# Kernel tuning notes

Hardware: AMD Instinct MI355X
Metric: run time of the kernel (lower is better)

The kernel has to match this reference:

```python
import jax, jax.numpy as jnp
import numpy as np

DIM = 512
NUM_HEADS = 8
HEAD_DIM = DIM // NUM_HEADS
SCALE = HEAD_DIM ** (-0.5)
EPS = 1e-12  # torch F.normalize eps


def setup_inputs() -> dict:
    key = jax.random.key(0)
    ks = jax.random.split(key, 6)
    B, C, H, W = 8, DIM, 64, 64
    x = jax.random.normal(ks[0], (B, C, H, W), dtype=jnp.float32)
    mask = jax.random.uniform(ks[1], (B, 1, H, W), dtype=jnp.float32)
    s = DIM ** -0.5
    Wq = jax.random.normal(ks[2], (DIM, DIM), dtype=jnp.float32) * s
    Wk = jax.random.normal(ks[3], (DIM, DIM), dtype=jnp.float32) * s
    Wv = jax.random.normal(ks[4], (DIM, DIM), dtype=jnp.float32) * s
    Wp = jax.random.normal(ks[5], (DIM, DIM), dtype=jnp.float32) * s
    return {"x": x, "mask": mask, "Wq": Wq, "Wk": Wk, "Wv": Wv, "Wp": Wp}


def _split_heads(t, B, HW):
    # [B, HW, C] -> [B, heads, head_dim, HW]
    return t.reshape(B, HW, NUM_HEADS, HEAD_DIM).transpose(0, 2, 3, 1)


def _l2norm(t):
    # torch F.normalize: x / max(||x||, eps) along last axis
    n = jnp.sqrt(jnp.sum(t * t, axis=-1, keepdims=True))
    return t / jnp.maximum(n, EPS)


def reference(x, mask, Wq, Wk, Wv, Wp):
    B, C, H, W = x.shape
    HW = H * W
    xm = x * mask                             # masked input for q, k
    # NCHW -> [B, HW, C]
    xt = x.transpose(0, 2, 3, 1).reshape(B, HW, C)
    xmt = xm.transpose(0, 2, 3, 1).reshape(B, HW, C)
    q = _split_heads(xmt @ Wq.T, B, HW)       # [B, h, d, HW]
    k = _split_heads(xmt @ Wk.T, B, HW)
    v = _split_heads(xt @ Wv.T, B, HW)
    q = _l2norm(q)
    k = _l2norm(k)
    # channel-wise attention: [B, h, d, d]
    attn = jnp.einsum('bhcn,bhdn->bhcd', q, k) * SCALE
    attn = jax.nn.softmax(attn, axis=-1)
    out = jnp.einsum('bhcd,bhdn->bhcn', attn, v)  # [B, h, d, HW]
    out = out.transpose(0, 3, 1, 2).reshape(B, HW, C)  # [B, HW, C]
    out = out @ Wp.T
    return out.reshape(B, H, W, C).transpose(0, 3, 1, 2)  # NCHW
```

## Files before the change

kernel.cpp:

```cpp
#include <hip/hip_runtime.h>
#include <math.h>

#define DIMC 512
#define HW 4096
#define SCALE 0.125f
#define EPSN 1e-12f

typedef __attribute__((ext_vector_type(8))) short bf16x8;
typedef __attribute__((ext_vector_type(4))) float f32x4;

__device__ __forceinline__ unsigned short f2bf(float f) {
    union { float f; unsigned int u; } v; v.f = f;
    unsigned int u = v.u;
    return (unsigned short)((u + 0x7fffu + ((u >> 16) & 1u)) >> 16);
}
__device__ __forceinline__ float bf2f(unsigned short h) {
    union { unsigned int u; float f; } v; v.u = ((unsigned int)h) << 16;
    return v.f;
}

union Pack8 { int4 v; unsigned short u[8]; };

__device__ __forceinline__ void gload_lds16(const unsigned short* src, char* ldst) {
    __builtin_amdgcn_global_load_lds(
        (const __attribute__((address_space(1))) void*)src,
        (__attribute__((address_space(3))) void*)ldst, 16, 0, 0);
}

__global__ __launch_bounds__(256) void convert_w(
    const float* __restrict__ Wq, const float* __restrict__ Wk,
    unsigned short* __restrict__ Wb)
{
    int i = (blockIdx.x * 256 + threadIdx.x) * 4;
    const float* s = (i < 262144) ? Wq : Wk;
    int off = i & 262143;
    float4 v4 = *(const float4*)(s + off);
    ushort4 o;
    o.x = f2bf(v4.x); o.y = f2bf(v4.y); o.z = f2bf(v4.z); o.w = f2bf(v4.w);
    *(ushort4*)(Wb + i) = o;
}

__global__ __launch_bounds__(256) void wvt_conv(
    const float* __restrict__ Wv, unsigned short* __restrict__ WvT)
{
    const int cp0 = blockIdx.y * 64;
    const int c30 = blockIdx.x * 64;
    __shared__ unsigned short sT[64][65];
    const int t = threadIdx.x;
    #pragma unroll
    for (int i = 0; i < 4; ++i) {
        int ch = t + i * 256;
        int r = ch >> 4, col4 = (ch & 15) * 4;
        float4 v4 = *(const float4*)(Wv + (size_t)(cp0 + r) * DIMC + c30 + col4);
        sT[r][col4 + 0] = f2bf(v4.x); sT[r][col4 + 1] = f2bf(v4.y);
        sT[r][col4 + 2] = f2bf(v4.z); sT[r][col4 + 3] = f2bf(v4.w);
    }
    __syncthreads();
    #pragma unroll
    for (int i = 0; i < 2; ++i) {
        int ch = t + i * 256;
        int n = ch >> 3, cc = (ch & 7) * 8;
        Pack8 pk;
        #pragma unroll
        for (int e = 0; e < 8; ++e) pk.u[e] = sT[cc + e][n];
        *(int4*)(WvT + (size_t)(c30 + n) * DIMC + cp0 + cc) = pk.v;
    }
}

__global__ __launch_bounds__(256) void prep_x(
    const float* __restrict__ x, const float* __restrict__ mask,
    unsigned short* __restrict__ xT, unsigned short* __restrict__ xmb)
{
    const int b  = blockIdx.z;
    const int c0 = blockIdx.y * 64;
    const int n0 = blockIdx.x * 64;
    __shared__ unsigned short sT[64][65];
    const int t = threadIdx.x;
    #pragma unroll
    for (int i = 0; i < 4; ++i) {
        int ch = t + i * 256;
        int r = ch >> 4, col4 = (ch & 15) * 4;
        float4 v4 = *(const float4*)(x + ((size_t)b * DIMC + c0 + r) * HW + n0 + col4);
        sT[r][col4 + 0] = f2bf(v4.x); sT[r][col4 + 1] = f2bf(v4.y);
        sT[r][col4 + 2] = f2bf(v4.z); sT[r][col4 + 3] = f2bf(v4.w);
        float4 mv = *(const float4*)(mask + (size_t)b * HW + n0 + col4);
        ushort4 xm;
        xm.x = f2bf(v4.x * mv.x); xm.y = f2bf(v4.y * mv.y);
        xm.z = f2bf(v4.z * mv.z); xm.w = f2bf(v4.w * mv.w);
        *(ushort4*)(xmb + ((size_t)b * DIMC + c0 + r) * HW + n0 + col4) = xm;
    }
    __syncthreads();
    #pragma unroll
    for (int i = 0; i < 2; ++i) {
        int ch = t + i * 256;
        int n = ch >> 3, cc = (ch & 7) * 8;
        Pack8 pk;
        #pragma unroll
        for (int e = 0; e < 8; ++e) pk.u[e] = sT[cc + e][n];
        *(int4*)(xT + ((size_t)b * HW + n0 + n) * DIMC + c0 + cc) = pk.v;
    }
}

__global__ __launch_bounds__(256) void gram_mfma(
    const unsigned short* __restrict__ xmb, unsigned short* __restrict__ G)
{
    const int b   = blockIdx.z;
    const int cA0 = blockIdx.y * 64;
    const int cB0 = blockIdx.x * 128;
    const unsigned short* A = xmb + (size_t)b * DIMC * HW + (size_t)cA0 * HW;
    const unsigned short* B = xmb + (size_t)b * DIMC * HW + (size_t)cB0 * HW;

    __shared__ __align__(16) char sm[49152];

    const int t = threadIdx.x, lane = t & 63, w = t >> 6;
    const int wm = w >> 1, wn = w & 1;
    const int rsub = lane >> 3;
    const int srccol = ((lane & 7) ^ rsub) << 3;

    f32x4 zero = {0.f, 0.f, 0.f, 0.f};
    f32x4 acc[2][4];
    #pragma unroll
    for (int m = 0; m < 2; ++m)
        #pragma unroll
        for (int n = 0; n < 4; ++n) acc[m][n] = zero;

    #define STAGE_G(buf, c0)                                                  \
        {                                                                     \
            char* dst = sm + (buf) * 24576;                                   \
            _Pragma("unroll")                                                 \
            for (int i = 0; i < 2; ++i) {                                     \
                int ii = w * 2 + i;                                           \
                gload_lds16(A + (size_t)(ii * 8 + rsub) * HW + (c0) + srccol, \
                            dst + ii * 1024);                                 \
            }                                                                 \
            _Pragma("unroll")                                                 \
            for (int i = 0; i < 4; ++i) {                                     \
                int ii = w * 4 + i;                                           \
                gload_lds16(B + (size_t)(ii * 8 + rsub) * HW + (c0) + srccol, \
                            dst + 8192 + ii * 1024);                          \
            }                                                                 \
        }

    STAGE_G(0, 0);
    int cur = 0;
    for (int c0 = 0; c0 < HW; c0 += 64) {
        __syncthreads();
        if (c0 + 64 < HW) STAGE_G(cur ^ 1, c0 + 64);
        const char* sA = sm + cur * 24576;
        const char* sB = sA + 8192;
        #pragma unroll
        for (int s = 0; s < 2; ++s) {
            bf16x8 af[2], bfr[4];
            #pragma unroll
            for (int m = 0; m < 2; ++m) {
                int r = wm * 32 + m * 16 + (lane & 15);
                int byte = r * 128 + s * 64 + ((lane >> 4) << 4);
                byte ^= (r & 7) << 4;
                af[m] = *(const bf16x8*)(sA + byte);
            }
            #pragma unroll
            for (int n = 0; n < 4; ++n) {
                int r = wn * 64 + n * 16 + (lane & 15);
                int byte = r * 128 + s * 64 + ((lane >> 4) << 4);
                byte ^= (r & 7) << 4;
                bfr[n] = *(const bf16x8*)(sB + byte);
            }
            #pragma unroll
            for (int m = 0; m < 2; ++m)
                #pragma unroll
                for (int n = 0; n < 4; ++n)
                    acc[m][n] = __builtin_amdgcn_mfma_f32_16x16x32_bf16(
                        af[m], bfr[n], acc[m][n], 0, 0, 0);
        }
        cur ^= 1;
    }
    #undef STAGE_G

    unsigned short* st = (unsigned short*)sm;
    __syncthreads();
    #pragma unroll
    for (int m = 0; m < 2; ++m)
        #pragma unroll
        for (int n = 0; n < 4; ++n)
            #pragma unroll
            for (int r4 = 0; r4 < 4; ++r4) {
                int jl = wm * 32 + m * 16 + ((lane >> 4) << 2) + r4;
                int nl = wn * 64 + n * 16 + (lane & 15);
                st[jl * 136 + nl] = f2bf(acc[m][n][r4]);
            }
    __syncthreads();
    #pragma unroll
    for (int it = 0; it < 4; ++it) {
        int idx = t + it * 256, jl = idx >> 4, l16 = idx & 15;
        int4 pv = *(int4*)((char*)sm + jl * 272 + l16 * 16);
        *(int4*)(G + ((size_t)b * DIMC + cA0 + jl) * DIMC + cB0 + l16 * 8) = pv;
    }
}

__global__ __launch_bounds__(256) void gemm_nn_128(
    const unsigned short* __restrict__ Ag, size_t aBatch,
    const unsigned short* __restrict__ Bg, size_t bBatch,
    unsigned short* __restrict__ Cg, size_t cBatch)
{
    const int b  = blockIdx.z;
    const int j0 = blockIdx.y * 128;
    const int n0 = blockIdx.x * 128;
    const unsigned short* A = Ag + (size_t)b * aBatch + (size_t)j0 * DIMC;
    const unsigned short* B = Bg + (size_t)b * bBatch + (size_t)n0 * DIMC;

    __shared__ __align__(16) char sm[65536];

    const int t = threadIdx.x, lane = t & 63, w = t >> 6;
    const int wm = w >> 1, wn = w & 1;
    const int rsub = lane >> 3;
    const int srccol = ((lane & 7) ^ rsub) << 3;

    f32x4 zero = {0.f, 0.f, 0.f, 0.f};
    f32x4 acc[4][4];
    #pragma unroll
    for (int m = 0; m < 4; ++m)
        #pragma unroll
        for (int n = 0; n < 4; ++n) acc[m][n] = zero;

    #define STAGE_NN(buf, c0)                                                   \
        {                                                                       \
            char* dst = sm + (buf) * 32768;                                     \
            _Pragma("unroll")                                                   \
            for (int i = 0; i < 4; ++i) {                                       \
                int ii = w * 4 + i;                                             \
                gload_lds16(A + (size_t)(ii * 8 + rsub) * DIMC + (c0) + srccol, \
                            dst + ii * 1024);                                   \
                gload_lds16(B + (size_t)(ii * 8 + rsub) * DIMC + (c0) + srccol, \
                            dst + 16384 + ii * 1024);                           \
            }                                                                   \
        }

    STAGE_NN(0, 0);
    int cur = 0;
    for (int c0 = 0; c0 < DIMC; c0 += 64) {
        __syncthreads();
        if (c0 + 64 < DIMC) STAGE_NN(cur ^ 1, c0 + 64);
        const char* sA = sm + cur * 32768;
        const char* sB = sA + 16384;
        #pragma unroll
        for (int s = 0; s < 2; ++s) {
            bf16x8 af[4], bfr[4];
            #pragma unroll
            for (int m = 0; m < 4; ++m) {
                int r = wm * 64 + m * 16 + (lane & 15);
                int byte = r * 128 + s * 64 + ((lane >> 4) << 4);
                byte ^= (r & 7) << 4;
                af[m] = *(const bf16x8*)(sA + byte);
            }
            #pragma unroll
            for (int n = 0; n < 4; ++n) {
                int r = wn * 64 + n * 16 + (lane & 15);
                int byte = r * 128 + s * 64 + ((lane >> 4) << 4);
                byte ^= (r & 7) << 4;
                bfr[n] = *(const bf16x8*)(sB + byte);
            }
            #pragma unroll
            for (int m = 0; m < 4; ++m)
                #pragma unroll
                for (int n = 0; n < 4; ++n)
                    acc[m][n] = __builtin_amdgcn_mfma_f32_16x16x32_bf16(
                        af[m], bfr[n], acc[m][n], 0, 0, 0);
        }
        cur ^= 1;
    }
    #undef STAGE_NN

    unsigned short* st = (unsigned short*)sm;
    __syncthreads();
    #pragma unroll
    for (int m = 0; m < 4; ++m)
        #pragma unroll
        for (int n = 0; n < 4; ++n)
            #pragma unroll
            for (int r4 = 0; r4 < 4; ++r4) {
                int jl = wm * 64 + m * 16 + ((lane >> 4) << 2) + r4;
                int nl = wn * 64 + n * 16 + (lane & 15);
                st[jl * 136 + nl] = f2bf(acc[m][n][r4]);
            }
    __syncthreads();
    #pragma unroll
    for (int it = 0; it < 8; ++it) {
        int idx = t + it * 256, jl = idx >> 4, l16 = idx & 15;
        int4 pv = *(int4*)((char*)sm + jl * 272 + l16 * 16);
        *(int4*)(Cg + (size_t)b * cBatch + (size_t)(j0 + jl) * DIMC + n0 + l16 * 8) = pv;
    }
}

__global__ __launch_bounds__(256) void sumsq_dot(
    const unsigned short* __restrict__ TU, const unsigned short* __restrict__ Wb,
    float* __restrict__ sumsq)
{
    const int row  = blockIdx.x * 4 + (threadIdx.x >> 6);
    const int lane = threadIdx.x & 63;
    const int b = row >> 10, jj = row & 1023;
    Pack8 a, wv;
    a.v  = *(const int4*)(TU + ((size_t)b * 1024 + jj) * DIMC + lane * 8);
    wv.v = *(const int4*)(Wb + (size_t)jj * DIMC + lane * 8);
    float s = 0.f;
    #pragma unroll
    for (int e = 0; e < 8; ++e) s = fmaf(bf2f(a.u[e]), bf2f(wv.u[e]), s);
    #pragma unroll
    for (int o = 32; o > 0; o >>= 1) s += __shfl_down(s, o, 64);
    if (lane == 0)
        sumsq[(jj >> 9) * 4096 + b * DIMC + (jj & 511)] = s;
}

__global__ __launch_bounds__(256) void s_softmax(
    const unsigned short* __restrict__ TU, const unsigned short* __restrict__ Wb,
    const float* __restrict__ sumsq, float* __restrict__ attn)
{
    const int bh = blockIdx.x;
    const int b = bh >> 3, h = bh & 7;
    const unsigned short* A = TU + ((size_t)b * 1024 + h * 64) * DIMC;
    const unsigned short* B = Wb + 262144 + (size_t)(h * 64) * DIMC;

    __shared__ __align__(16) char sm[32768];
    __shared__ float sS[64][65];
    __shared__ float srk[64];

    const int t = threadIdx.x, lane = t & 63, w = t >> 6;
    const int wm = w >> 1, wn = w & 1;
    const int rsub = lane >> 3;
    const int srccol = ((lane & 7) ^ rsub) << 3;

    f32x4 zero = {0.f, 0.f, 0.f, 0.f};
    f32x4 acc[2][2];
    #pragma unroll
    for (int m = 0; m < 2; ++m)
        #pragma unroll
        for (int n = 0; n < 2; ++n) acc[m][n] = zero;

    #define STAGE_S(buf, c0)                                                    \
        {                                                                       \
            char* dst = sm + (buf) * 16384;                                     \
            _Pragma("unroll")                                                   \
            for (int i = 0; i < 2; ++i) {                                       \
                int ii = w * 2 + i;                                             \
                gload_lds16(A + (size_t)(ii * 8 + rsub) * DIMC + (c0) + srccol, \
                            dst + ii * 1024);                                   \
                gload_lds16(B + (size_t)(ii * 8 + rsub) * DIMC + (c0) + srccol, \
                            dst + 8192 + ii * 1024);                            \
            }                                                                   \
        }

    STAGE_S(0, 0);
    int cur = 0;
    for (int c0 = 0; c0 < DIMC; c0 += 64) {
        __syncthreads();
        if (c0 + 64 < DIMC) STAGE_S(cur ^ 1, c0 + 64);
        const char* sA = sm + cur * 16384;
        const char* sB = sA + 8192;
        #pragma unroll
        for (int s = 0; s < 2; ++s) {
            bf16x8 aq[2], bk[2];
            #pragma unroll
            for (int m = 0; m < 2; ++m) {
                int r = wm * 32 + m * 16 + (lane & 15);
                int byte = r * 128 + s * 64 + ((lane >> 4) << 4);
                byte ^= (r & 7) << 4;
                aq[m] = *(const bf16x8*)(sA + byte);
            }
            #pragma unroll
            for (int n = 0; n < 2; ++n) {
                int r = wn * 32 + n * 16 + (lane & 15);
                int byte = r * 128 + s * 64 + ((lane >> 4) << 4);
                byte ^= (r & 7) << 4;
                bk[n] = *(const bf16x8*)(sB + byte);
            }
            #pragma unroll
            for (int m = 0; m < 2; ++m)
                #pragma unroll
                for (int n = 0; n < 2; ++n)
                    acc[m][n] = __builtin_amdgcn_mfma_f32_16x16x32_bf16(
                        aq[m], bk[n], acc[m][n], 0, 0, 0);
        }
        cur ^= 1;
    }
    #undef STAGE_S

    #pragma unroll
    for (int m = 0; m < 2; ++m)
        #pragma unroll
        for (int n = 0; n < 2; ++n)
            #pragma unroll
            for (int r4 = 0; r4 < 4; ++r4) {
                int r = wm * 32 + m * 16 + ((lane >> 4) << 2) + r4;
                int c = wn * 32 + n * 16 + (lane & 15);
                sS[r][c] = acc[m][n][r4];
            }
    if (t < 64)
        srk[t] = 1.0f / fmaxf(sqrtf(sumsq[4096 + b * DIMC + h * 64 + t]), EPSN);
    __syncthreads();

    const int r = t >> 2;
    const int p = t & 3;
    const float rq = 1.0f / fmaxf(sqrtf(sumsq[b * DIMC + h * 64 + r]), EPSN);
    float row[16];
    #pragma unroll
    for (int c = 0; c < 16; ++c)
        row[c] = sS[r][p * 16 + c] * SCALE * rq * srk[p * 16 + c];
    float mx = row[0];
    #pragma unroll
    for (int c = 1; c < 16; ++c) mx = fmaxf(mx, row[c]);
    mx = fmaxf(mx, __shfl_xor(mx, 1, 4));
    mx = fmaxf(mx, __shfl_xor(mx, 2, 4));
    float sum = 0.f;
    #pragma unroll
    for (int c = 0; c < 16; ++c) { row[c] = __expf(row[c] - mx); sum += row[c]; }
    sum += __shfl_xor(sum, 1, 4);
    sum += __shfl_xor(sum, 2, 4);
    const float inv = 1.0f / sum;
    float* Ao = attn + ((size_t)bh << 12) + r * 64 + p * 16;
    #pragma unroll
    for (int c4 = 0; c4 < 4; ++c4) {
        float4 o = make_float4(row[c4*4+0]*inv, row[c4*4+1]*inv,
                               row[c4*4+2]*inv, row[c4*4+3]*inv);
        *(float4*)(Ao + c4 * 4) = o;
    }
}

__global__ __launch_bounds__(256) void build_wp2(
    const float* __restrict__ Wp, const float* __restrict__ attn,
    unsigned short* __restrict__ Wp2b)
{
    const int jt = blockIdx.x;
    const int h  = blockIdx.y;
    const int b  = blockIdx.z;

    __shared__ float sA[64][64];
    __shared__ float sW[64][64];

    const int t = threadIdx.x;
    {
        const float* A = attn + ((size_t)(b * 8 + h) << 12);
        for (int i = t * 4; i < 4096; i += 1024)
            *(float4*)&sA[0][i] = *(const float4*)(A + i);
    }
    {
        const int j  = t >> 2;
        const int c0 = (t & 3) * 16;
        #pragma unroll
        for (int i = 0; i < 4; ++i) {
            float4 w4 = *(const float4*)(Wp + (size_t)(jt * 64 + j) * DIMC + h * 64 + c0 + i * 4);
            sW[c0 + i * 4 + 0][j] = w4.x; sW[c0 + i * 4 + 1][j] = w4.y;
            sW[c0 + i * 4 + 2][j] = w4.z; sW[c0 + i * 4 + 3][j] = w4.w;
        }
    }
    __syncthreads();

    const int tx = t & 15, ty = t >> 4;
    float acc[4][4] = {};
    #pragma unroll 16
    for (int c = 0; c < 64; ++c) {
        float wf[4], af[4];
        #pragma unroll
        for (int i = 0; i < 4; ++i) { wf[i] = sW[c][ty * 4 + i]; af[i] = sA[c][tx * 4 + i]; }
        #pragma unroll
        for (int r = 0; r < 4; ++r)
            #pragma unroll
            for (int cc = 0; cc < 4; ++cc)
                acc[r][cc] = fmaf(wf[r], af[cc], acc[r][cc]);
    }

    unsigned short* O = Wp2b + ((size_t)b * DIMC + jt * 64 + ty * 4) * DIMC + h * 64 + tx * 4;
    #pragma unroll
    for (int r = 0; r < 4; ++r) {
        ushort4 o4;
        o4.x = f2bf(acc[r][0]); o4.y = f2bf(acc[r][1]);
        o4.z = f2bf(acc[r][2]); o4.w = f2bf(acc[r][3]);
        *(ushort4*)(O + (size_t)r * DIMC) = o4;
    }
}

__global__ __launch_bounds__(256) void final_mfma(
    const unsigned short* __restrict__ Wfb, const unsigned short* __restrict__ xT,
    float* __restrict__ out)
{
    const int b  = blockIdx.z;
    const int j0 = blockIdx.y * 128;
    const int n0 = blockIdx.x * 128;
    const unsigned short* A = Wfb + (size_t)b * DIMC * DIMC + (size_t)j0 * DIMC;
    const unsigned short* B = xT + (size_t)b * HW * DIMC + (size_t)n0 * DIMC;

    __shared__ __align__(16) char sm[65536];

    const int t = threadIdx.x, lane = t & 63, w = t >> 6;
    const int wm = w >> 1, wn = w & 1;
    const int rsub = lane >> 3;
    const int srccol = ((lane & 7) ^ rsub) << 3;

    f32x4 zero = {0.f, 0.f, 0.f, 0.f};
    f32x4 acc[4][4];
    #pragma unroll
    for (int m = 0; m < 4; ++m)
        #pragma unroll
        for (int n = 0; n < 4; ++n) acc[m][n] = zero;

    #define STAGE_FIN(buf, c0)                                                  \
        {                                                                       \
            char* dst = sm + (buf) * 32768;                                     \
            _Pragma("unroll")                                                   \
            for (int i = 0; i < 4; ++i) {                                       \
                int ii = w * 4 + i;                                             \
                gload_lds16(A + (size_t)(ii * 8 + rsub) * DIMC + (c0) + srccol, \
                            dst + ii * 1024);                                   \
                gload_lds16(B + (size_t)(ii * 8 + rsub) * DIMC + (c0) + srccol, \
                            dst + 16384 + ii * 1024);                           \
            }                                                                   \
        }

    STAGE_FIN(0, 0);
    int cur = 0;
    for (int c0 = 0; c0 < DIMC; c0 += 64) {
        __syncthreads();
        if (c0 + 64 < DIMC) STAGE_FIN(cur ^ 1, c0 + 64);
        const char* sA = sm + cur * 32768;
        const char* sB = sA + 16384;
        #pragma unroll
        for (int s = 0; s < 2; ++s) {
            bf16x8 af[4], bfr[4];
            #pragma unroll
            for (int m = 0; m < 4; ++m) {
                int r = wm * 64 + m * 16 + (lane & 15);
                int byte = r * 128 + s * 64 + ((lane >> 4) << 4);
                byte ^= (r & 7) << 4;
                af[m] = *(const bf16x8*)(sA + byte);
            }
            #pragma unroll
            for (int n = 0; n < 4; ++n) {
                int r = wn * 64 + n * 16 + (lane & 15);
                int byte = r * 128 + s * 64 + ((lane >> 4) << 4);
                byte ^= (r & 7) << 4;
                bfr[n] = *(const bf16x8*)(sB + byte);
            }
            #pragma unroll
            for (int m = 0; m < 4; ++m)
                #pragma unroll
                for (int n = 0; n < 4; ++n)
                    acc[m][n] = __builtin_amdgcn_mfma_f32_16x16x32_bf16(
                        af[m], bfr[n], acc[m][n], 0, 0, 0);
        }
        cur ^= 1;
    }
    #undef STAGE_FIN

    #pragma unroll
    for (int m = 0; m < 4; ++m)
        #pragma unroll
        for (int r4 = 0; r4 < 4; ++r4) {
            int j = j0 + wm * 64 + m * 16 + ((lane >> 4) << 2) + r4;
            size_t rowbase = ((size_t)b * DIMC + j) * HW + n0 + wn * 64 + (lane & 15);
            #pragma unroll
            for (int n = 0; n < 4; ++n)
                out[rowbase + n * 16] = acc[m][n][r4];
        }
}

extern "C" void kernel_launch(void* const* d_in, const int* in_sizes, int n_in,
                              void* d_out, int out_size, void* d_ws, size_t ws_size,
                              hipStream_t stream)
{
    const float* x    = (const float*)d_in[0];
    const float* mask = (const float*)d_in[1];
    const float* Wq   = (const float*)d_in[2];
    const float* Wk   = (const float*)d_in[3];
    const float* Wv   = (const float*)d_in[4];
    const float* Wp   = (const float*)d_in[5];
    float* out = (float*)d_out;
    char* wsb = (char*)d_ws;

    unsigned short* xT   = (unsigned short*)(wsb + 0);
    unsigned short* xmb  = (unsigned short*)(wsb + 67108864);
    unsigned short* Wb   = (unsigned short*)(wsb + 134217728);
    unsigned short* WvT  = (unsigned short*)(wsb + 135266304);
    unsigned short* G    = (unsigned short*)(wsb + 135790592);
    unsigned short* TU   = (unsigned short*)(wsb + 139984896);
    float* sumsq         = (float*)(wsb + 148373504);
    float* attn          = (float*)(wsb + 148406272);
    unsigned short* Wp2b = (unsigned short*)(wsb + 149454848);
    unsigned short* Wfb  = (unsigned short*)(wsb + 153649152);

    convert_w  <<<512,             256, 0, stream>>>(Wq, Wk, Wb);
    wvt_conv   <<<dim3(8, 8),      256, 0, stream>>>(Wv, WvT);
    prep_x     <<<dim3(64, 8, 8),  256, 0, stream>>>(x, mask, xT, xmb);
    gram_mfma  <<<dim3(4, 8, 8),   256, 0, stream>>>(xmb, G);
    gemm_nn_128<<<dim3(4, 8, 8),   256, 0, stream>>>(Wb, (size_t)0, G, (size_t)(DIMC*DIMC), TU, (size_t)(1024*DIMC));
    sumsq_dot  <<<2048,            256, 0, stream>>>(TU, Wb, sumsq);
    s_softmax  <<<64,              256, 0, stream>>>(TU, Wb, sumsq, attn);
    build_wp2  <<<dim3(8, 8, 8),   256, 0, stream>>>(Wp, attn, Wp2b);
    gemm_nn_128<<<dim3(4, 4, 8),   256, 0, stream>>>(Wp2b, (size_t)(DIMC*DIMC), WvT, (size_t)0, Wfb, (size_t)(DIMC*DIMC));
    final_mfma <<<dim3(32, 4, 8),  256, 0, stream>>>(Wfb, xT, out);
}
```

Baseline: 132.4 us.

## Split Gram-matrix reduction over HW into four partials with a reduce kernel

The Gram kernel now splits the 4096-long reduction dimension into four 1024-long chunks and enlarges the output tile to 128x128, giving 512 blocks instead of 256. Each block writes fp32 partial results, and a new reduce kernel sums the four partials and converts them to bf16. The aim is better occupancy of the compute units and more reuse of each loaded tile. The cost is an extra kernel launch, 32 MB of fp32 partial writes and reads, and uncoalesced per-element partial stores.

New measurement: 134.1 us. About the same (+1.3%).

```diff
diff --git a/kernel.cpp b/kernel.cpp
--- a/kernel.cpp
+++ b/kernel.cpp
@@ -102,15 +102,16 @@
 }
 
 __global__ __launch_bounds__(256) void gram_mfma(
-    const unsigned short* __restrict__ xmb, unsigned short* __restrict__ G)
-{
-    const int b   = blockIdx.z;
-    const int cA0 = blockIdx.y * 64;
+    const unsigned short* __restrict__ xmb, float* __restrict__ Gpart)
+{
+    const int b   = blockIdx.z & 7;
+    const int sp  = blockIdx.z >> 3;
+    const int cA0 = blockIdx.y * 128;
     const int cB0 = blockIdx.x * 128;
-    const unsigned short* A = xmb + (size_t)b * DIMC * HW + (size_t)cA0 * HW;
-    const unsigned short* B = xmb + (size_t)b * DIMC * HW + (size_t)cB0 * HW;
-
-    __shared__ __align__(16) char sm[49152];
+    const unsigned short* A = xmb + (size_t)b * DIMC * HW + (size_t)cA0 * HW + sp * 1024;
+    const unsigned short* B = xmb + (size_t)b * DIMC * HW + (size_t)cB0 * HW + sp * 1024;
+
+    __shared__ __align__(16) char sm[65536];
 
     const int t = threadIdx.x, lane = t & 63, w = t >> 6;
     const int wm = w >> 1, wn = w & 1;
@@ -118,42 +119,38 @@
     const int srccol = ((lane & 7) ^ rsub) << 3;
 
     f32x4 zero = {0.f, 0.f, 0.f, 0.f};
-    f32x4 acc[2][4];
-    #pragma unroll
-    for (int m = 0; m < 2; ++m)
+    f32x4 acc[4][4];
+    #pragma unroll
+    for (int m = 0; m < 4; ++m)
         #pragma unroll
         for (int n = 0; n < 4; ++n) acc[m][n] = zero;
 
     #define STAGE_G(buf, c0)                                                  \
         {                                                                     \
-            char* dst = sm + (buf) * 24576;                                   \
-            _Pragma("unroll")                                                 \
-            for (int i = 0; i < 2; ++i) {                                     \
-                int ii = w * 2 + i;                                           \
-                gload_lds16(A + (size_t)(ii * 8 + rsub) * HW + (c0) + srccol, \
-                            dst + ii * 1024);                                 \
-            }                                                                 \
+            char* dst = sm + (buf) * 32768;                                   \
             _Pragma("unroll")                                                 \
             for (int i = 0; i < 4; ++i) {                                     \
                 int ii = w * 4 + i;                                           \
+                gload_lds16(A + (size_t)(ii * 8 + rsub) * HW + (c0) + srccol, \
+                            dst + ii * 1024);                                 \
                 gload_lds16(B + (size_t)(ii * 8 + rsub) * HW + (c0) + srccol, \
-                            dst + 8192 + ii * 1024);                          \
+                            dst + 16384 + ii * 1024);                         \
             }                                                                 \
         }
 
     STAGE_G(0, 0);
     int cur = 0;
-    for (int c0 = 0; c0 < HW; c0 += 64) {
+    for (int c0 = 0; c0 < 1024; c0 += 64) {
         __syncthreads();
-        if (c0 + 64 < HW) STAGE_G(cur ^ 1, c0 + 64);
-        const char* sA = sm + cur * 24576;
-        const char* sB = sA + 8192;
+        if (c0 + 64 < 1024) STAGE_G(cur ^ 1, c0 + 64);
+        const char* sA = sm + cur * 32768;
+        const char* sB = sA + 16384;
         #pragma unroll
         for (int s = 0; s < 2; ++s) {
-            bf16x8 af[2], bfr[4];
-            #pragma unroll
-            for (int m = 0; m < 2; ++m) {
-                int r = wm * 32 + m * 16 + (lane & 15);
+            bf16x8 af[4], bfr[4];
+            #pragma unroll
+            for (int m = 0; m < 4; ++m) {
+                int r = wm * 64 + m * 16 + (lane & 15);
                 int byte = r * 128 + s * 64 + ((lane >> 4) << 4);
                 byte ^= (r & 7) << 4;
                 af[m] = *(const bf16x8*)(sA + byte);
@@ -166,7 +163,7 @@
                 bfr[n] = *(const bf16x8*)(sB + byte);
             }
             #pragma unroll
-            for (int m = 0; m < 2; ++m)
+            for (int m = 0; m < 4; ++m)
                 #pragma unroll
                 for (int n = 0; n < 4; ++n)
                     acc[m][n] = __builtin_amdgcn_mfma_f32_16x16x32_bf16(
@@ -176,25 +173,33 @@
     }
     #undef STAGE_G
 
-    unsigned short* st = (unsigned short*)sm;
-    __syncthreads();
-    #pragma unroll
-    for (int m = 0; m < 2; ++m)
-        #pragma unroll
-        for (int n = 0; n < 4; ++n)
-            #pragma unroll
-            for (int r4 = 0; r4 < 4; ++r4) {
-                int jl = wm * 32 + m * 16 + ((lane >> 4) << 2) + r4;
-                int nl = wn * 64 + n * 16 + (lane & 15);
-                st[jl * 136 + nl] = f2bf(acc[m][n][r4]);
-            }
-    __syncthreads();
-    #pragma unroll
-    for (int it = 0; it < 4; ++it) {
-        int idx = t + it * 256, jl = idx >> 4, l16 = idx & 15;
-        int4 pv = *(int4*)((char*)sm + jl * 272 + l16 * 16);
-        *(int4*)(G + ((size_t)b * DIMC + cA0 + jl) * DIMC + cB0 + l16 * 8) = pv;
-    }
+    float* O = Gpart + ((size_t)sp * 8 + b) * DIMC * DIMC;
+    #pragma unroll
+    for (int m = 0; m < 4; ++m)
+        #pragma unroll
+        for (int r4 = 0; r4 < 4; ++r4) {
+            int row = cA0 + wm * 64 + m * 16 + ((lane >> 4) << 2) + r4;
+            size_t rowbase = (size_t)row * DIMC + cB0 + wn * 64 + (lane & 15);
+            #pragma unroll
+            for (int n = 0; n < 4; ++n)
+                O[rowbase + n * 16] = acc[m][n][r4];
+        }
+}
+
+__global__ __launch_bounds__(256) void gram_reduce(
+    const float* __restrict__ Gpart, unsigned short* __restrict__ G)
+{
+    size_t i = ((size_t)blockIdx.x * 256 + threadIdx.x) * 4;
+    float4 a0 = *(const float4*)(Gpart + i);
+    float4 a1 = *(const float4*)(Gpart + 2097152 + i);
+    float4 a2 = *(const float4*)(Gpart + 4194304 + i);
+    float4 a3 = *(const float4*)(Gpart + 6291456 + i);
+    ushort4 o;
+    o.x = f2bf(a0.x + a1.x + a2.x + a3.x);
+    o.y = f2bf(a0.y + a1.y + a2.y + a3.y);
+    o.z = f2bf(a0.z + a1.z + a2.z + a3.z);
+    o.w = f2bf(a0.w + a1.w + a2.w + a3.w);
+    *(ushort4*)(G + i) = o;
 }
 
 __global__ __launch_bounds__(256) void gemm_nn_128(
@@ -584,11 +589,13 @@
     float* attn          = (float*)(wsb + 148406272);
     unsigned short* Wp2b = (unsigned short*)(wsb + 149454848);
     unsigned short* Wfb  = (unsigned short*)(wsb + 153649152);
+    float* Gpart         = (float*)(wsb + 157843456);
 
     convert_w  <<<512,             256, 0, stream>>>(Wq, Wk, Wb);
     wvt_conv   <<<dim3(8, 8),      256, 0, stream>>>(Wv, WvT);
     prep_x     <<<dim3(64, 8, 8),  256, 0, stream>>>(x, mask, xT, xmb);
-    gram_mfma  <<<dim3(4, 8, 8),   256, 0, stream>>>(xmb, G);
+    gram_mfma  <<<dim3(4, 4, 32),  256, 0, stream>>>(xmb, Gpart);
+    gram_reduce<<<2048,            256, 0, stream>>>(Gpart, G);
     gemm_nn_128<<<dim3(4, 8, 8),   256, 0, stream>>>(Wb, (size_t)0, G, (size_t)(DIMC*DIMC), TU, (size_t)(1024*DIMC));
     sumsq_dot  <<<2048,            256, 0, stream>>>(TU, Wb, sumsq);
     s_softmax  <<<64,              256, 0, stream>>>(TU, Wb, sumsq, attn);
```
